# Kernel tuning notes

Hardware: AMD Instinct MI355X
Metric: run time of the kernel (lower is better)

The kernel has to match this reference:

```python
import jax, jax.numpy as jnp
import numpy as np
from jax import lax

HFACTOR = 0.5


def setup_inputs() -> dict:
    key = jax.random.key(0)
    ks = jax.random.split(key, 10)
    B, T, D, K, C = 256, 128, 768, 74, 128
    feats = jax.random.normal(ks[0], (B, T, D), jnp.float32)
    attention_mask = jnp.ones((B, T), jnp.int32)
    labels = jax.random.randint(ks[1], (B, T), 0, K)
    cache = jax.random.normal(ks[2], (C, 128, K), jnp.float32)
    W1 = jax.random.normal(ks[3], (D, K), jnp.float32) * 0.02
    b1 = jnp.zeros((K,), jnp.float32)
    W2 = jax.random.normal(ks[4], (K, K), jnp.float32) * 0.1
    b2 = jnp.zeros((K,), jnp.float32)
    start_trans = jax.random.normal(ks[5], (K,), jnp.float32) * 0.1
    end_trans = jax.random.normal(ks[6], (K,), jnp.float32) * 0.1
    transitions = jax.random.normal(ks[7], (K, K), jnp.float32) * 0.1
    return dict(feats=feats, attention_mask=attention_mask, labels=labels,
                cache=cache, W1=W1, b1=b1, W2=W2, b2=b2,
                start_trans=start_trans, end_trans=end_trans,
                transitions=transitions)


def _crf_normalizer(em, mask, start, end, trans):
    # em: [T,B,K], mask: [T,B] bool -> log partition per batch [B]
    score0 = start[None, :] + em[0]
    def step(score, inp):
        e, m = inp
        nxt = jax.nn.logsumexp(score[:, :, None] + trans[None] + e[:, None, :], axis=1)
        return jnp.where(m[:, None], nxt, score), None
    score, _ = lax.scan(step, score0, (em[1:], mask[1:]))
    return jax.nn.logsumexp(score + end[None, :], axis=1)


def _crf_score(em, tags, mask, start, end, trans):
    # em: [T,B,K], tags: [T,B], mask: [T,B] -> gold path score [B]
    T, B, K = em.shape
    b = jnp.arange(B)
    score0 = start[tags[0]] + em[0, b, tags[0]]
    maskf = mask.astype(em.dtype)
    def step(carry, inp):
        score, prev = carry
        e, t, m = inp
        score = score + (trans[prev, t] + e[b, t]) * m
        return (score, t), None
    (score, _), _ = lax.scan(step, (score0, tags[0]), (em[1:], tags[1:], maskf[1:]))
    seq_ends = jnp.sum(mask.astype(jnp.int32), axis=0) - 1  # [B]
    last = tags[seq_ends, b]
    return score + end[last]


def _viterbi(em, mask, start, end, trans):
    # em: [T,B,K], mask: [T,B] bool -> best tag sequence [B,T]
    T, B, K = em.shape
    b = jnp.arange(B)
    score0 = start[None, :] + em[0]
    def fwd(score, inp):
        e, m = inp
        br = score[:, :, None] + trans[None]          # [B,K_prev,K_cur]
        idx = jnp.argmax(br, axis=1)                  # [B,K]
        nxt = jnp.max(br, axis=1) + e
        return jnp.where(m[:, None], nxt, score), idx
    score, hist = lax.scan(fwd, score0, (em[1:], mask[1:]))  # hist: [T-1,B,K]
    best_last = jnp.argmax(score + end[None, :], axis=1)     # [B]
    def back(cur, inp):
        h, m = inp                                    # h: [B,K], m: [B]
        cur_t = jnp.where(m, h[b, cur], best_last)
        return cur_t, cur_t
    _, tags_rev = lax.scan(back, best_last, (hist[::-1], mask[1:][::-1]))
    tags = jnp.concatenate([tags_rev[::-1], best_last[None]], axis=0)  # [T,B]
    return tags.T


def reference(feats, attention_mask, labels, cache, W1, b1, W2, b2,
              start_trans, end_trans, transitions):
    T = feats.shape[1]
    logits = feats @ W1 + b1                                   # [B,T,K]
    c = cache[:, :T]                                           # [C,T,K]
    sim = jnp.einsum('pjk,qjk->pq', logits, c)                 # [B,C]
    p = jax.nn.softmax(sim, axis=1)
    h = jnp.einsum('ij,jkl->ikl', p, c)                        # [B,T,K]
    new_logits = (logits + h * HFACTOR) @ W2 + b2              # [B,T,K]
    em = jnp.transpose(new_logits, (1, 0, 2))                  # [T,B,K]
    mask_t = attention_mask.T.astype(bool)                     # [T,B]
    prob = _viterbi(em, mask_t, start_trans, end_trans, transitions)
    num = _crf_score(em, labels.T, mask_t, start_trans, end_trans, transitions)
    den = _crf_normalizer(em, mask_t, start_trans, end_trans, transitions)
    loss = -jnp.mean(num - den)                                # torchcrf reduction='mean', negated
    return (prob, loss)
```

## Files before the change

kernel.cpp:

```cpp
#include <hip/hip_runtime.h>

#define B_ 256
#define T_ 128
#define D_ 768
#define K_ 74
#define C_ 128
#define TK_ 9472
#define BT_ 32768
#define EMS_ 18944

#define LGKM_BARRIER() do { \
    asm volatile("s_waitcnt lgkmcnt(0)" ::: "memory"); \
    __builtin_amdgcn_s_barrier(); \
    __builtin_amdgcn_sched_barrier(0); \
} while (0)

__global__ void pad_weights(const float* __restrict__ W1, const float* __restrict__ W2,
                            float* __restrict__ W1q, float* __restrict__ W2q)
{
    int idx = blockIdx.x * 256 + threadIdx.x;
    if (idx < 4 * 768 * 20) {
        int nq = idx / (768 * 20); int rem = idx - nq * (768 * 20);
        int k = rem / 20, j = rem - k * 20;
        int c = nq * 19 + j;
        W1q[idx] = (j < 19 && c < 74) ? W1[k * 74 + c] : 0.f;
    }
    if (idx < 4 * 74 * 20) {
        int nq = idx / (74 * 20); int rem = idx - nq * (74 * 20);
        int k = rem / 20, j = rem - k * 20;
        int c = nq * 19 + j;
        W2q[idx] = (j < 19 && c < 74) ? W2[k * 74 + c] : 0.f;
    }
}

__global__ __launch_bounds__(256) void gemm_logits_part(const float* __restrict__ feats,
    const float* __restrict__ W1q, float* __restrict__ outA, float* __restrict__ outB)
{
    int orig = blockIdx.x;
    int vb = (orig & 7) * 128 + (orig >> 3);
    int rb = vb >> 3, nq = (vb >> 1) & 3, ks = vb & 1;
    int tid = threadIdx.x;
    int r = rb * 256 + tid;
    int c0 = nq * 19;
    const float* frow = feats + (size_t)r * 768 + ks * 384;
    const float* wq = W1q + nq * (768 * 20) + ks * 384 * 20;
    float acc[20];
    #pragma unroll
    for (int j = 0; j < 20; ++j) acc[j] = 0.f;

    for (int k0 = 0; k0 < 384; k0 += 16) {
        float4 a[4];
        #pragma unroll
        for (int q = 0; q < 4; ++q) a[q] = *(const float4*)(frow + k0 + 4 * q);
        #pragma unroll
        for (int u = 0; u < 16; ++u) {
            float av = ((const float*)a)[u];
            const float* wr = wq + (k0 + u) * 20;
            #pragma unroll
            for (int j = 0; j < 20; ++j) acc[j] += av * wr[j];
        }
    }
    float* P = ks ? outB : outA;
    #pragma unroll
    for (int j = 0; j < 19; ++j) {
        int c = c0 + j;
        if (c < 74) P[(size_t)r * 74 + c] = acc[j];
    }
}

__global__ void logits_sum(const float* __restrict__ Bp, const float* __restrict__ b1,
                           float* __restrict__ logits)
{
    int idx = blockIdx.x * 256 + threadIdx.x;
    int r = idx / 74; int c = idx - r * 74;
    logits[idx] = logits[idx] + Bp[idx] + b1[c];
}

__global__ __launch_bounds__(256) void sim_partial(const float* __restrict__ logits,
    const float* __restrict__ cache, float* __restrict__ part)
{
    __shared__ float As[74][68];
    __shared__ float Bs[74][68];
    int tid = threadIdx.x;
    int tx = tid & 15, ty = tid >> 4;
    int bid = blockIdx.x;
    int jc = bid >> 3;
    int mt = (bid >> 1) & 3;
    int nt = bid & 1;
    int p0 = mt * 64, q0 = nt * 64;
    float acc[4][4] = {};
    for (int jj = 0; jj < 2; ++jj) {
        int j = jc * 2 + jj;
        for (int it = 0; it < 19; ++it) {
            int lin = it * 256 + tid;
            if (lin < 64 * 74) {
                int r = lin / 74, ik = lin - r * 74;
                As[ik][r] = logits[(p0 + r) * TK_ + j * 74 + ik];
                Bs[ik][r] = cache[(q0 + r) * TK_ + j * 74 + ik];
            }
        }
        __syncthreads();
        for (int ik = 0; ik < 74; ++ik) {
            float4 a = *(const float4*)&As[ik][4 * tx];
            float4 b = *(const float4*)&Bs[ik][4 * ty];
            const float* ap = (const float*)&a;
            const float* bp = (const float*)&b;
            #pragma unroll
            for (int i = 0; i < 4; ++i)
                #pragma unroll
                for (int q = 0; q < 4; ++q) acc[i][q] += ap[i] * bp[q];
        }
        __syncthreads();
    }
    #pragma unroll
    for (int i = 0; i < 4; ++i)
        #pragma unroll
        for (int q = 0; q < 4; ++q)
            part[jc * (B_ * C_) + (p0 + 4 * tx + i) * C_ + q0 + 4 * ty + q] = acc[i][q];
}

__global__ void sim_reduce(const float* __restrict__ part, float* __restrict__ sim)
{
    int idx = blockIdx.x * 256 + threadIdx.x;
    float s = 0.f;
    for (int jc = 0; jc < 64; ++jc) s += part[jc * (B_ * C_) + idx];
    sim[idx] = s;
}

__global__ void softmax128(const float* __restrict__ sim, float* __restrict__ p)
{
    __shared__ float red[128];
    int q = threadIdx.x, row = blockIdx.x;
    float v = sim[row * 128 + q];
    red[q] = v; __syncthreads();
    for (int s = 64; s > 0; s >>= 1) { if (q < s) red[q] = fmaxf(red[q], red[q + s]); __syncthreads(); }
    float m = red[0]; __syncthreads();
    float e = expf(v - m);
    red[q] = e; __syncthreads();
    for (int s = 64; s > 0; s >>= 1) { if (q < s) red[q] += red[q + s]; __syncthreads(); }
    float sum = red[0];
    p[row * 128 + q] = e / sum;
}

__global__ __launch_bounds__(256) void gemm_h_y(const float* __restrict__ pmat,
    const float* __restrict__ cache, const float* __restrict__ logits, float* __restrict__ y)
{
    __shared__ float As[64][68];
    __shared__ float Bs[64][68];
    int tid = threadIdx.x;
    int tx = tid & 15, ty = tid >> 4;
    int orig = blockIdx.x;
    int vb = (orig & 7) * 74 + (orig >> 3);
    int mt = vb / 148, nt = vb - mt * 148;
    int r0 = mt * 64, n0 = nt * 64;
    float acc[4][4] = {};
    #pragma unroll
    for (int s = 0; s < 2; ++s) {
        #pragma unroll
        for (int it = 0; it < 16; ++it) {
            int lin = it * 256 + tid;
            int r = lin >> 6, kk = lin & 63;
            As[kk][r] = pmat[(r0 + r) * 128 + s * 64 + kk];
        }
        #pragma unroll
        for (int it = 0; it < 16; ++it) {
            int lin = it * 256 + tid;
            int kk = lin >> 6, c = lin & 63;
            Bs[kk][c] = cache[(s * 64 + kk) * TK_ + n0 + c];
        }
        __syncthreads();
        for (int kk = 0; kk < 64; ++kk) {
            float4 a = *(const float4*)&As[kk][4 * tx];
            float4 b = *(const float4*)&Bs[kk][4 * ty];
            const float* ap = (const float*)&a;
            const float* bp = (const float*)&b;
            #pragma unroll
            for (int i = 0; i < 4; ++i)
                #pragma unroll
                for (int j = 0; j < 4; ++j) acc[i][j] += ap[i] * bp[j];
        }
        __syncthreads();
    }
    #pragma unroll
    for (int i = 0; i < 4; ++i) {
        int r = r0 + 4 * tx + i;
        #pragma unroll
        for (int j = 0; j < 4; ++j) {
            int n = n0 + 4 * ty + j;
            y[r * TK_ + n] = logits[r * TK_ + n] + 0.5f * acc[i][j];
        }
    }
}

__global__ __launch_bounds__(256) void gemm_em(const float* __restrict__ y,
    const float* __restrict__ W2q, const float* __restrict__ b2, float* __restrict__ em)
{
    int orig = blockIdx.x;
    int vb = (orig & 7) * 64 + (orig >> 3);
    int rb = vb >> 2, nq = vb & 3;
    int tid = threadIdx.x;
    int r = rb * 256 + tid;
    int c0 = nq * 19;
    const float* wq = W2q + nq * (74 * 20);
    const float* yrow = y + (size_t)r * 74;
    float acc[20];
    #pragma unroll
    for (int j = 0; j < 20; ++j) acc[j] = 0.f;
    #pragma unroll 1
    for (int k0 = 0; k0 < 74; k0 += 2) {
        float2 a = *(const float2*)(yrow + k0);
        const float* ap = (const float*)&a;
        #pragma unroll
        for (int u = 0; u < 2; ++u) {
            const float* wr = wq + (k0 + u) * 20;
            #pragma unroll
            for (int j = 0; j < 20; ++j) acc[j] += ap[u] * wr[j];
        }
    }
    int b = r >> 7, t = r & 127;
    #pragma unroll
    for (int j = 0; j < 19; ++j) {
        int c = c0 + j;
        if (c < 74) em[t * EMS_ + b * 74 + c] = acc[j] + b2[c];
    }
}

__global__ __launch_bounds__(256) void crf_scan(const float* __restrict__ em,
    const int* __restrict__ mask_, const float* __restrict__ startv,
    const float* __restrict__ endv, const float* __restrict__ trans,
    float* __restrict__ out_tags, float* __restrict__ den)
{
    __shared__ float transS[74 * 74];
    __shared__ float scoreS[2][88];
    __shared__ float EscS[2][88] __attribute__((aligned(16)));
    __shared__ float pv[3][74];
    __shared__ int   pi[3][74];
    __shared__ unsigned char histS[127 * 74];
    __shared__ float tagsS[128];
    __shared__ float Ms[2];
    __shared__ int   flagU[2];
    __shared__ int   maskS[128];
    int tid = threadIdx.x;
    bool isV = blockIdx.x < 256;
    int b = isV ? blockIdx.x : (blockIdx.x - 256);

    for (int i = tid; i < 74 * 74; i += 256) transS[i] = trans[i];
    if (tid < 128) maskS[tid] = mask_[b * 128 + tid];
    if (tid >= 74 && tid < 88) {
        scoreS[0][tid] = -3.0e38f; scoreS[1][tid] = -3.0e38f;
        EscS[0][tid] = 0.f;        EscS[1][tid] = 0.f;
    }
    if (tid < 74) scoreS[0][tid] = startv[tid] + em[b * 74 + tid];
    __syncthreads();

    int ch = (tid < 74) ? 0 : (tid < 148 ? 1 : 2);
    int kp = tid - ch * 74;
    int cbase = ch * 28;
    float tr[28];
    if (tid < 222) {
        #pragma unroll
        for (int j = 0; j < 28; ++j) {
            int kk = cbase + j;
            tr[j] = (kk < 74) ? transS[kk * 74 + kp] : -1.0e30f;
        }
    }
    int cur = 0;

    float eA = 0.f, eB = 0.f;
    if (tid < 74) {
        eA = em[1 * EMS_ + b * 74 + tid];
        eB = em[2 * EMS_ + b * 74 + tid];
    }

    if (isV) {
        for (int t = 1; t < 128; ++t) {
            float eC = 0.f;
            if (tid < 74 && t + 2 < 128) eC = em[(t + 2) * EMS_ + b * 74 + tid];
            if (tid < 222) {
                float mA = -3.0e38f; int iA = cbase;
                float mB = -3.0e38f; int iB = cbase + 12;
                #pragma unroll
                for (int jj = 0; jj < 3; ++jj) {
                    float4 s4 = *(const float4*)&scoreS[cur][cbase + 4 * jj];
                    const float* sp = (const float*)&s4;
                    #pragma unroll
                    for (int u = 0; u < 4; ++u) {
                        float v = sp[u] + tr[4 * jj + u];
                        if (v > mA) { mA = v; iA = cbase + 4 * jj + u; }
                    }
                }
                #pragma unroll
                for (int jj = 3; jj < 7; ++jj) {
                    float4 s4 = *(const float4*)&scoreS[cur][cbase + 4 * jj];
                    const float* sp = (const float*)&s4;
                    #pragma unroll
                    for (int u = 0; u < 4; ++u) {
                        float v = sp[u] + tr[4 * jj + u];
                        if (v > mB) { mB = v; iB = cbase + 4 * jj + u; }
                    }
                }
                float m; int mi;
                if (mB > mA) { m = mB; mi = iB; } else { m = mA; mi = iA; }
                pv[ch][kp] = m; pi[ch][kp] = mi;
            }
            LGKM_BARRIER();
            int mk = maskS[t];
            if (tid < 74) {
                float m0 = pv[0][tid]; int i0 = pi[0][tid];
                if (pv[1][tid] > m0) { m0 = pv[1][tid]; i0 = pi[1][tid]; }
                if (pv[2][tid] > m0) { m0 = pv[2][tid]; i0 = pi[2][tid]; }
                histS[(t - 1) * 74 + tid] = (unsigned char)i0;
                scoreS[cur ^ 1][tid] = mk ? (m0 + eA) : scoreS[cur][tid];
            }
            LGKM_BARRIER();
            cur ^= 1;
            eA = eB; eB = eC;
        }
        if (tid == 0) {
            float bm = scoreS[cur][0] + endv[0]; int bi = 0;
            for (int k = 1; k < 74; ++k) {
                float v = scoreS[cur][k] + endv[k];
                if (v > bm) { bm = v; bi = k; }
            }
            int curk = bi;
            tagsS[127] = (float)bi;
            for (int ti = 126; ti >= 0; --ti) {
                int mk = maskS[ti + 1];
                curk = mk ? (int)histS[ti * 74 + curk] : bi;
                tagsS[ti] = (float)curk;
            }
        }
        __syncthreads();
        if (tid < 128) out_tags[b * 128 + tid] = tagsS[tid];
    } else {
        if (tid < 222) {
            #pragma unroll
            for (int j = 0; j < 28; ++j) tr[j] = __expf(tr[j]);
        }
        float v0 = (tid < 74) ? scoreS[0][tid] : -3.0e38f;
        float M;
        if (tid < 128) {
            #pragma unroll
            for (int off = 32; off > 0; off >>= 1) v0 = fmaxf(v0, __shfl_xor(v0, off));
            if ((tid & 63) == 0) Ms[tid >> 6] = v0;
        }
        __syncthreads();
        M = fmaxf(Ms[0], Ms[1]);
        if (tid < 74) EscS[0][tid] = __expf(scoreS[0][tid] - M);
        int count = 0;
        LGKM_BARRIER();
        for (int t = 1; t < 128; ++t) {
            float eC = 0.f;
            if (tid < 74 && t + 2 < 128) eC = em[(t + 2) * EMS_ + b * 74 + tid];
            if (tid < 222) {
                float s0 = 0.f, s1 = 0.f, s2 = 0.f, s3 = 0.f;
                #pragma unroll
                for (int jj = 0; jj < 7; ++jj) {
                    float4 E4 = *(const float4*)&EscS[cur][cbase + 4 * jj];
                    s0 += E4.x * tr[4 * jj + 0];
                    s1 += E4.y * tr[4 * jj + 1];
                    s2 += E4.z * tr[4 * jj + 2];
                    s3 += E4.w * tr[4 * jj + 3];
                }
                pv[ch][kp] = (s0 + s1) + (s2 + s3);
            }
            LGKM_BARRIER();
            int mk = maskS[t];
            int over = 0, notsmall = 0;
            if (tid < 74) {
                float u = pv[0][tid] + pv[1][tid] + pv[2][tid];
                float un = u * __expf(eA);
                float En = mk ? un : EscS[cur][tid];
                EscS[cur ^ 1][tid] = En;
                over = (En > 0x1p64f) ? 1 : 0;
                notsmall = (En >= 0x1p-32f) ? 1 : 0;
            }
            int wOver = __any(over) ? 1 : 0;
            int wNs = __any(notsmall) ? 2 : 0;
            if ((tid & 63) == 0 && tid < 128) flagU[tid >> 6] = wOver | wNs;
            LGKM_BARRIER();
            cur ^= 1;
            int fl = flagU[0] | flagU[1];
            if (fl & 1) {
                if (tid < 74) EscS[cur][tid] *= 0x1p-64f;
                count++;
                LGKM_BARRIER();
            } else if (!(fl & 2)) {
                if (tid < 74) EscS[cur][tid] *= 0x1p64f;
                count--;
                LGKM_BARRIER();
            }
            eA = eB; eB = eC;
        }
        if (tid == 0) {
            float s = 0.f;
            for (int k = 0; k < 74; ++k) s += EscS[cur][k] * __expf(endv[k]);
            den[b] = M + (float)count * 44.36141955583650f + __logf(s);
        }
    }
}

__global__ __launch_bounds__(128) void loss_partial(const float* __restrict__ em,
    const int* __restrict__ labels, const int* __restrict__ mask_,
    const float* __restrict__ startv, const float* __restrict__ endv,
    const float* __restrict__ den, const float* __restrict__ trans, float* __restrict__ nd)
{
    __shared__ float cs[2];
    __shared__ int ms[2];
    int b = blockIdx.x, t = threadIdx.x;
    int lab = labels[b * 128 + t];
    int mk = mask_[b * 128 + t];
    float contrib;
    if (t == 0) {
        contrib = startv[lab] + em[b * 74 + lab];
    } else {
        int labp = labels[b * 128 + t - 1];
        contrib = mk ? (trans[labp * 74 + lab] + em[t * EMS_ + b * 74 + lab]) : 0.f;
    }
    float c = contrib; int m = mk;
    #pragma unroll
    for (int off = 32; off > 0; off >>= 1) {
        c += __shfl_xor(c, off);
        m += __shfl_xor(m, off);
    }
    if ((t & 63) == 0) { cs[t >> 6] = c; ms[t >> 6] = m; }
    __syncthreads();
    if (t == 0) {
        float num = cs[0] + cs[1];
        int msum = ms[0] + ms[1];
        int last = labels[b * 128 + msum - 1];
        num += endv[last];
        nd[b] = num - den[b];
    }
}

__global__ void loss_final(const float* __restrict__ nd, float* __restrict__ out_loss)
{
    __shared__ float red[256];
    int i = threadIdx.x;
    red[i] = nd[i];
    __syncthreads();
    for (int s = 128; s > 0; s >>= 1) { if (i < s) red[i] += red[i + s]; __syncthreads(); }
    if (i == 0) out_loss[0] = -(red[0] / 256.f);
}

extern "C" void kernel_launch(void* const* d_in, const int* in_sizes, int n_in,
                              void* d_out, int out_size, void* d_ws, size_t ws_size,
                              hipStream_t stream)
{
    const float* feats  = (const float*)d_in[0];
    const int*   amask  = (const int*)d_in[1];
    const int*   labels = (const int*)d_in[2];
    const float* cache  = (const float*)d_in[3];
    const float* W1     = (const float*)d_in[4];
    const float* b1     = (const float*)d_in[5];
    const float* W2     = (const float*)d_in[6];
    const float* b2     = (const float*)d_in[7];
    const float* startv = (const float*)d_in[8];
    const float* endv   = (const float*)d_in[9];
    const float* trans  = (const float*)d_in[10];

    float* ws     = (float*)d_ws;
    float* logits = ws;
    float* y      = ws + 2424832;
    float* em     = ws + 4849664;
    float* scratch= ws + 7274496;
    float* sim    = ws + 8323072;
    float* p      = ws + 8355840;
    float* den    = ws + 8388608;
    float* nd     = ws + 8388864;
    float* W2q    = ws + 8389120;
    float* W1q    = scratch;
    float* part   = y;
    float* out_tags = (float*)d_out;
    float* out_loss = (float*)d_out + 32768;

    hipLaunchKernelGGL(pad_weights,      dim3(240),  dim3(256), 0, stream, W1, W2, W1q, W2q);
    hipLaunchKernelGGL(gemm_logits_part, dim3(1024), dim3(256), 0, stream, feats, W1q, logits, y);
    hipLaunchKernelGGL(logits_sum,       dim3(9472), dim3(256), 0, stream, y, b1, logits);
    hipLaunchKernelGGL(sim_partial,      dim3(512),  dim3(256), 0, stream, logits, cache, part);
    hipLaunchKernelGGL(sim_reduce,       dim3(128),  dim3(256), 0, stream, part, sim);
    hipLaunchKernelGGL(softmax128,       dim3(256),  dim3(128), 0, stream, sim, p);
    hipLaunchKernelGGL(gemm_h_y,         dim3(592),  dim3(256), 0, stream, p, cache, logits, y);
    hipLaunchKernelGGL(gemm_em,          dim3(512),  dim3(256), 0, stream, y, W2q, b2, em);
    hipLaunchKernelGGL(crf_scan,         dim3(512),  dim3(256), 0, stream, em, amask, startv, endv, trans, out_tags, den);
    hipLaunchKernelGGL(loss_partial,     dim3(256),  dim3(128), 0, stream, em, labels, amask, startv, endv, den, trans, nd);
    hipLaunchKernelGGL(loss_final,       dim3(1),    dim3(256), 0, stream, nd, out_loss);
}
```

Measured before the change: 253.6 us.

## Reduce CRF scan partials with wave shuffles and split logits GEMM K three ways

The CRF scan now uses 320 threads, with four lanes per destination tag each covering 20 source tags. Their partial max/argmax or sum is combined with xor shuffles instead of a shared-memory round trip, which removes one barrier per time step. Each owner lane keeps its previous score in a register. The logits GEMM also splits K into three chunks instead of two, launching more blocks for better occupancy, at the cost of an extra partial buffer to read in the sum kernel.

After: 273.9 us. +8.0%, slower.

```diff
diff --git a/kernel.cpp b/kernel.cpp
--- a/kernel.cpp
+++ b/kernel.cpp
@@ -34,21 +34,23 @@
 }
 
 __global__ __launch_bounds__(256) void gemm_logits_part(const float* __restrict__ feats,
-    const float* __restrict__ W1q, float* __restrict__ outA, float* __restrict__ outB)
+    const float* __restrict__ W1q, float* __restrict__ P0, float* __restrict__ P1,
+    float* __restrict__ P2)
 {
     int orig = blockIdx.x;
-    int vb = (orig & 7) * 128 + (orig >> 3);
-    int rb = vb >> 3, nq = (vb >> 1) & 3, ks = vb & 1;
+    int vb = (orig & 7) * 192 + (orig >> 3);
+    int rb = vb / 12; int rem = vb - rb * 12;
+    int nq = rem / 3, ks = rem - nq * 3;
     int tid = threadIdx.x;
     int r = rb * 256 + tid;
     int c0 = nq * 19;
-    const float* frow = feats + (size_t)r * 768 + ks * 384;
-    const float* wq = W1q + nq * (768 * 20) + ks * 384 * 20;
+    const float* frow = feats + (size_t)r * 768 + ks * 256;
+    const float* wq = W1q + nq * (768 * 20) + ks * 256 * 20;
     float acc[20];
     #pragma unroll
     for (int j = 0; j < 20; ++j) acc[j] = 0.f;
 
-    for (int k0 = 0; k0 < 384; k0 += 16) {
+    for (int k0 = 0; k0 < 256; k0 += 16) {
         float4 a[4];
         #pragma unroll
         for (int q = 0; q < 4; ++q) a[q] = *(const float4*)(frow + k0 + 4 * q);
@@ -60,7 +62,7 @@
             for (int j = 0; j < 20; ++j) acc[j] += av * wr[j];
         }
     }
-    float* P = ks ? outB : outA;
+    float* P = (ks == 0) ? P0 : ((ks == 1) ? P1 : P2);
     #pragma unroll
     for (int j = 0; j < 19; ++j) {
         int c = c0 + j;
@@ -68,12 +70,12 @@
     }
 }
 
-__global__ void logits_sum(const float* __restrict__ Bp, const float* __restrict__ b1,
-                           float* __restrict__ logits)
+__global__ void logits_sum(const float* __restrict__ P1, const float* __restrict__ P2,
+                           const float* __restrict__ b1, float* __restrict__ logits)
 {
     int idx = blockIdx.x * 256 + threadIdx.x;
     int r = idx / 74; int c = idx - r * 74;
-    logits[idx] = logits[idx] + Bp[idx] + b1[c];
+    logits[idx] = logits[idx] + P1[idx] + P2[idx] + b1[c];
 }
 
 __global__ __launch_bounds__(256) void sim_partial(const float* __restrict__ logits,
@@ -225,92 +227,95 @@
     }
 }
 
-__global__ __launch_bounds__(256) void crf_scan(const float* __restrict__ em,
+__global__ __launch_bounds__(320) void crf_scan(const float* __restrict__ em,
     const int* __restrict__ mask_, const float* __restrict__ startv,
     const float* __restrict__ endv, const float* __restrict__ trans,
     float* __restrict__ out_tags, float* __restrict__ den)
 {
     __shared__ float transS[74 * 74];
-    __shared__ float scoreS[2][88];
-    __shared__ float EscS[2][88] __attribute__((aligned(16)));
-    __shared__ float pv[3][74];
-    __shared__ int   pi[3][74];
+    __shared__ float scoreS[2][80] __attribute__((aligned(16)));
+    __shared__ float EscS[2][80] __attribute__((aligned(16)));
     __shared__ unsigned char histS[127 * 74];
     __shared__ float tagsS[128];
     __shared__ float Ms[2];
-    __shared__ int   flagU[2];
+    __shared__ int   flagU[5];
     __shared__ int   maskS[128];
     int tid = threadIdx.x;
     bool isV = blockIdx.x < 256;
     int b = isV ? blockIdx.x : (blockIdx.x - 256);
 
-    for (int i = tid; i < 74 * 74; i += 256) transS[i] = trans[i];
+    for (int i = tid; i < 74 * 74; i += 320) transS[i] = trans[i];
     if (tid < 128) maskS[tid] = mask_[b * 128 + tid];
-    if (tid >= 74 && tid < 88) {
+    if (tid >= 74 && tid < 80) {
         scoreS[0][tid] = -3.0e38f; scoreS[1][tid] = -3.0e38f;
         EscS[0][tid] = 0.f;        EscS[1][tid] = 0.f;
     }
-    if (tid < 74) scoreS[0][tid] = startv[tid] + em[b * 74 + tid];
     __syncthreads();
 
-    int ch = (tid < 74) ? 0 : (tid < 148 ? 1 : 2);
-    int kp = tid - ch * 74;
-    int cbase = ch * 28;
-    float tr[28];
-    if (tid < 222) {
-        #pragma unroll
-        for (int j = 0; j < 28; ++j) {
-            int kk = cbase + j;
-            tr[j] = (kk < 74) ? transS[kk * 74 + kp] : -1.0e30f;
-        }
-    }
+    int w = tid >> 6, lane = tid & 63;
+    int destL = lane >> 2, subsrc = lane & 3;
+    int dest = w * 16 + destL;
+    bool isD = dest < 74;
+    bool isOwner = (subsrc == 0) && isD;
+    int kbase = subsrc * 20;
+
+    float tr[20];
+    #pragma unroll
+    for (int j = 0; j < 20; ++j) {
+        int k = kbase + j;
+        tr[j] = (isD && k < 74) ? transS[k * 74 + dest] : -1.0e30f;
+    }
+
+    float prev = 0.f, eA = 0.f, eB = 0.f;
+    if (isOwner) {
+        prev = startv[dest] + em[b * 74 + dest];
+        scoreS[0][dest] = prev;
+        eA = em[1 * EMS_ + b * 74 + dest];
+        eB = em[2 * EMS_ + b * 74 + dest];
+    }
+    __syncthreads();
     int cur = 0;
-
-    float eA = 0.f, eB = 0.f;
-    if (tid < 74) {
-        eA = em[1 * EMS_ + b * 74 + tid];
-        eB = em[2 * EMS_ + b * 74 + tid];
-    }
 
     if (isV) {
         for (int t = 1; t < 128; ++t) {
             float eC = 0.f;
-            if (tid < 74 && t + 2 < 128) eC = em[(t + 2) * EMS_ + b * 74 + tid];
-            if (tid < 222) {
-                float mA = -3.0e38f; int iA = cbase;
-                float mB = -3.0e38f; int iB = cbase + 12;
+            if (isOwner && t + 2 < 128) eC = em[(t + 2) * EMS_ + b * 74 + dest];
+            float mA = -3.0e38f; int iA = kbase;
+            float mB = -3.0e38f; int iB = kbase + 8;
+            #pragma unroll
+            for (int jj = 0; jj < 2; ++jj) {
+                float4 s4 = *(const float4*)&scoreS[cur][kbase + 4 * jj];
+                const float* sp = (const float*)&s4;
                 #pragma unroll
-                for (int jj = 0; jj < 3; ++jj) {
-                    float4 s4 = *(const float4*)&scoreS[cur][cbase + 4 * jj];
-                    const float* sp = (const float*)&s4;
-                    #pragma unroll
-                    for (int u = 0; u < 4; ++u) {
-                        float v = sp[u] + tr[4 * jj + u];
-                        if (v > mA) { mA = v; iA = cbase + 4 * jj + u; }
-                    }
+                for (int u = 0; u < 4; ++u) {
+                    float v = sp[u] + tr[4 * jj + u];
+                    if (v > mA) { mA = v; iA = kbase + 4 * jj + u; }
                 }
+            }
+            #pragma unroll
+            for (int jj = 2; jj < 5; ++jj) {
+                float4 s4 = *(const float4*)&scoreS[cur][kbase + 4 * jj];
+                const float* sp = (const float*)&s4;
                 #pragma unroll
-                for (int jj = 3; jj < 7; ++jj) {
-                    float4 s4 = *(const float4*)&scoreS[cur][cbase + 4 * jj];
-                    const float* sp = (const float*)&s4;
-                    #pragma unroll
-                    for (int u = 0; u < 4; ++u) {
-                        float v = sp[u] + tr[4 * jj + u];
-                        if (v > mB) { mB = v; iB = cbase + 4 * jj + u; }
-                    }
+                for (int u = 0; u < 4; ++u) {
+                    float v = sp[u] + tr[4 * jj + u];
+                    if (v > mB) { mB = v; iB = kbase + 4 * jj + u; }
                 }
-                float m; int mi;
-                if (mB > mA) { m = mB; mi = iB; } else { m = mA; mi = iA; }
-                pv[ch][kp] = m; pi[ch][kp] = mi;
-            }
-            LGKM_BARRIER();
+            }
+            float m; int mi;
+            if (mB > mA) { m = mB; mi = iB; } else { m = mA; mi = iA; }
+            #pragma unroll
+            for (int off = 1; off <= 2; off <<= 1) {
+                float vo = __shfl_xor(m, off);
+                int io = __shfl_xor(mi, off);
+                if (vo > m || (vo == m && io < mi)) { m = vo; mi = io; }
+            }
             int mk = maskS[t];
-            if (tid < 74) {
-                float m0 = pv[0][tid]; int i0 = pi[0][tid];
-                if (pv[1][tid] > m0) { m0 = pv[1][tid]; i0 = pi[1][tid]; }
-                if (pv[2][tid] > m0) { m0 = pv[2][tid]; i0 = pi[2][tid]; }
-                histS[(t - 1) * 74 + tid] = (unsigned char)i0;
-                scoreS[cur ^ 1][tid] = mk ? (m0 + eA) : scoreS[cur][tid];
+            if (isOwner) {
+                histS[(t - 1) * 74 + dest] = (unsigned char)mi;
+                float snew = mk ? (m + eA) : prev;
+                scoreS[cur ^ 1][dest] = snew;
+                prev = snew;
             }
             LGKM_BARRIER();
             cur ^= 1;
@@ -333,60 +338,57 @@
         __syncthreads();
         if (tid < 128) out_tags[b * 128 + tid] = tagsS[tid];
     } else {
-        if (tid < 222) {
-            #pragma unroll
-            for (int j = 0; j < 28; ++j) tr[j] = __expf(tr[j]);
-        }
+        #pragma unroll
+        for (int j = 0; j < 20; ++j) tr[j] = __expf(tr[j]);
         float v0 = (tid < 74) ? scoreS[0][tid] : -3.0e38f;
-        float M;
         if (tid < 128) {
             #pragma unroll
             for (int off = 32; off > 0; off >>= 1) v0 = fmaxf(v0, __shfl_xor(v0, off));
             if ((tid & 63) == 0) Ms[tid >> 6] = v0;
         }
         __syncthreads();
-        M = fmaxf(Ms[0], Ms[1]);
-        if (tid < 74) EscS[0][tid] = __expf(scoreS[0][tid] - M);
+        float M = fmaxf(Ms[0], Ms[1]);
+        float Eprev = 0.f;
+        if (isOwner) { Eprev = __expf(prev - M); EscS[0][dest] = Eprev; }
         int count = 0;
         LGKM_BARRIER();
         for (int t = 1; t < 128; ++t) {
             float eC = 0.f;
-            if (tid < 74 && t + 2 < 128) eC = em[(t + 2) * EMS_ + b * 74 + tid];
-            if (tid < 222) {
-                float s0 = 0.f, s1 = 0.f, s2 = 0.f, s3 = 0.f;
-                #pragma unroll
-                for (int jj = 0; jj < 7; ++jj) {
-                    float4 E4 = *(const float4*)&EscS[cur][cbase + 4 * jj];
-                    s0 += E4.x * tr[4 * jj + 0];
-                    s1 += E4.y * tr[4 * jj + 1];
-                    s2 += E4.z * tr[4 * jj + 2];
-                    s3 += E4.w * tr[4 * jj + 3];
-                }
-                pv[ch][kp] = (s0 + s1) + (s2 + s3);
-            }
-            LGKM_BARRIER();
+            if (isOwner && t + 2 < 128) eC = em[(t + 2) * EMS_ + b * 74 + dest];
+            float s0 = 0.f, s1 = 0.f, s2 = 0.f, s3 = 0.f;
+            #pragma unroll
+            for (int jj = 0; jj < 5; ++jj) {
+                float4 E4 = *(const float4*)&EscS[cur][kbase + 4 * jj];
+                s0 += E4.x * tr[4 * jj + 0];
+                s1 += E4.y * tr[4 * jj + 1];
+                s2 += E4.z * tr[4 * jj + 2];
+                s3 += E4.w * tr[4 * jj + 3];
+            }
+            float u = (s0 + s1) + (s2 + s3);
+            u += __shfl_xor(u, 1);
+            u += __shfl_xor(u, 2);
             int mk = maskS[t];
             int over = 0, notsmall = 0;
-            if (tid < 74) {
-                float u = pv[0][tid] + pv[1][tid] + pv[2][tid];
-                float un = u * __expf(eA);
-                float En = mk ? un : EscS[cur][tid];
-                EscS[cur ^ 1][tid] = En;
+            if (isOwner) {
+                float En = mk ? (u * __expf(eA)) : Eprev;
+                EscS[cur ^ 1][dest] = En;
+                Eprev = En;
                 over = (En > 0x1p64f) ? 1 : 0;
                 notsmall = (En >= 0x1p-32f) ? 1 : 0;
             }
-            int wOver = __any(over) ? 1 : 0;
-            int wNs = __any(notsmall) ? 2 : 0;
-            if ((tid & 63) == 0 && tid < 128) flagU[tid >> 6] = wOver | wNs;
+            int wf = (__any(over) ? 1 : 0) | (__any(notsmall) ? 2 : 0);
+            if (lane == 0) flagU[w] = wf;
             LGKM_BARRIER();
             cur ^= 1;
-            int fl = flagU[0] | flagU[1];
-            if (fl & 1) {
-                if (tid < 74) EscS[cur][tid] *= 0x1p-64f;
+            int flO = 0, flN = 0;
+            #pragma unroll
+            for (int q = 0; q < 5; ++q) { flO |= flagU[q] & 1; flN |= flagU[q] & 2; }
+            if (flO) {
+                if (isOwner) { Eprev *= 0x1p-64f; EscS[cur][dest] = Eprev; }
                 count++;
                 LGKM_BARRIER();
-            } else if (!(fl & 2)) {
-                if (tid < 74) EscS[cur][tid] *= 0x1p64f;
+            } else if (!flN) {
+                if (isOwner) { Eprev *= 0x1p64f; EscS[cur][dest] = Eprev; }
                 count--;
                 LGKM_BARRIER();
             }
@@ -476,14 +478,14 @@
     float* out_loss = (float*)d_out + 32768;
 
     hipLaunchKernelGGL(pad_weights,      dim3(240),  dim3(256), 0, stream, W1, W2, W1q, W2q);
-    hipLaunchKernelGGL(gemm_logits_part, dim3(1024), dim3(256), 0, stream, feats, W1q, logits, y);
-    hipLaunchKernelGGL(logits_sum,       dim3(9472), dim3(256), 0, stream, y, b1, logits);
+    hipLaunchKernelGGL(gemm_logits_part, dim3(1536), dim3(256), 0, stream, feats, W1q, logits, y, em);
+    hipLaunchKernelGGL(logits_sum,       dim3(9472), dim3(256), 0, stream, y, em, b1, logits);
     hipLaunchKernelGGL(sim_partial,      dim3(512),  dim3(256), 0, stream, logits, cache, part);
     hipLaunchKernelGGL(sim_reduce,       dim3(128),  dim3(256), 0, stream, part, sim);
     hipLaunchKernelGGL(softmax128,       dim3(256),  dim3(128), 0, stream, sim, p);
     hipLaunchKernelGGL(gemm_h_y,         dim3(592),  dim3(256), 0, stream, p, cache, logits, y);
     hipLaunchKernelGGL(gemm_em,          dim3(512),  dim3(256), 0, stream, y, W2q, b2, em);
-    hipLaunchKernelGGL(crf_scan,         dim3(512),  dim3(256), 0, stream, em, amask, startv, endv, trans, out_tags, den);
+    hipLaunchKernelGGL(crf_scan,         dim3(512),  dim3(320), 0, stream, em, amask, startv, endv, trans, out_tags, den);
     hipLaunchKernelGGL(loss_partial,     dim3(256),  dim3(128), 0, stream, em, labels, amask, startv, endv, den, trans, nd);
     hipLaunchKernelGGL(loss_final,       dim3(1),    dim3(256), 0, stream, nd, out_loss);
 }
```
